# Performance work log

Measured on AMD Instinct MI355X. Metric: run time of the kernel, lower is better.

Reference implementation:

```python
import jax, jax.numpy as jnp
import numpy as np

N_NODES = 100000
N_EDGES = 1600000
N_GRAPHS = 128
IN_FEATS = 128
H2 = 128
N_CLASSES = 64


def setup_inputs() -> dict:
    key = jax.random.key(0)
    ks = jax.random.split(key, 12)
    return {
        "feat1": jax.random.normal(ks[0], (N_NODES, IN_FEATS), jnp.float32),
        "feat2": jax.random.normal(ks[1], (N_NODES, IN_FEATS), jnp.float32),
        "src1": jax.random.randint(ks[2], (N_EDGES,), 0, N_NODES),
        "dst1": jax.random.randint(ks[3], (N_EDGES,), 0, N_NODES),
        "gid1": jnp.sort(jax.random.randint(ks[4], (N_NODES,), 0, N_GRAPHS)),
        "src2": jax.random.randint(ks[5], (N_EDGES,), 0, N_NODES),
        "dst2": jax.random.randint(ks[6], (N_EDGES,), 0, N_NODES),
        "gid2": jnp.sort(jax.random.randint(ks[7], (N_NODES,), 0, N_GRAPHS)),
        "W": jax.random.normal(ks[8], (IN_FEATS, H2), jnp.float32) * 0.05,
        "b": jax.random.normal(ks[9], (H2,), jnp.float32) * 0.05,
        "Wc": jax.random.normal(ks[10], (H2, N_CLASSES), jnp.float32) * 0.05,
        "bc": jax.random.normal(ks[11], (N_CLASSES,), jnp.float32) * 0.05,
    }


def _gcn_branch(feat, src, dst, gid, W, b, Wc, bc):
    n = feat.shape[0]
    ones = jnp.ones(src.shape[0], feat.dtype)
    # DGL GraphConv norm='both': D_out^{-1/2} on src side, D_in^{-1/2} on dst side
    deg_out = jnp.clip(jax.ops.segment_sum(ones, src, num_segments=n), 1.0)
    deg_in = jnp.clip(jax.ops.segment_sum(ones, dst, num_segments=n), 1.0)
    h = feat * (deg_out ** -0.5)[:, None]
    h = h @ W  # project before aggregation (same linear math, fewer edge FLOPs)
    agg = jax.ops.segment_sum(h[src], dst, num_segments=n)  # [N, H2]
    h = agg * (deg_in ** -0.5)[:, None] + b
    # F.normalize (L2, dim=1, eps=1e-12) -> sigmoid -> relu (identity after sigmoid)
    h = h / jnp.clip(jnp.linalg.norm(h, axis=1, keepdims=True), 1e-12)
    h = jax.nn.relu(jax.nn.sigmoid(h))
    # dropout(0.3) omitted for deterministic reference (identity)
    # mean_nodes per graph
    hg = jax.ops.segment_sum(h, gid, num_segments=N_GRAPHS)
    cnt = jnp.clip(jax.ops.segment_sum(jnp.ones(n, h.dtype), gid, num_segments=N_GRAPHS), 1.0)
    hg = hg / cnt[:, None]
    return hg @ Wc + bc  # [G, C]


def reference(feat1, feat2, src1, dst1, gid1, src2, dst2, gid2, W, b, Wc, bc):
    h1 = _gcn_branch(feat1, src1, dst1, gid1, W, b, Wc, bc)
    h2 = _gcn_branch(feat2, src2, dst2, gid2, W, b, Wc, bc)
    # torch F.pairwise_distance: ||x1 - x2 + eps||_2 with eps=1e-6
    return jnp.linalg.norm(h1 - h2 + 1e-6, axis=1)
```

## Files before the change

### kernel.cpp

```cpp
#include <hip/hip_runtime.h>
#include <hip/hip_fp16.h>
#include <math.h>

#define F 128
#define C 64
#define G 128
#define KMAX 512
#define P1CH 2048
#define CAPB 4608

typedef _Float16 f16x8 __attribute__((ext_vector_type(8)));
typedef float f32x4 __attribute__((ext_vector_type(4)));

__device__ __forceinline__ void atomicAddF(float* p, float v) {
  __hip_atomic_fetch_add(p, v, __ATOMIC_RELAXED, __HIP_MEMORY_SCOPE_AGENT);
}

__global__ __launch_bounds__(256) void fscale_kernel(
    const float* __restrict__ feat1, const float* __restrict__ feat2,
    const float* __restrict__ dno1, const float* __restrict__ dno2,
    unsigned char* __restrict__ fs1, unsigned char* __restrict__ fs2, int N) {
  const float* feat = blockIdx.y ? feat2 : feat1;
  const float* dno = blockIdx.y ? dno2 : dno1;
  unsigned char* fs = blockIdx.y ? fs2 : fs1;
  int i = blockIdx.x * blockDim.x + threadIdx.x;
  if (i >= N * (F / 8)) return;
  int node = i >> 4;
  float dn = dno[node];
  float4 v0 = ((const float4*)feat)[i * 2];
  float4 v1 = ((const float4*)feat)[i * 2 + 1];
  int w0 = __builtin_amdgcn_cvt_pk_fp8_f32(v0.x * dn, v0.y * dn, 0, false);
  w0 = __builtin_amdgcn_cvt_pk_fp8_f32(v0.z * dn, v0.w * dn, w0, true);
  int w1 = __builtin_amdgcn_cvt_pk_fp8_f32(v1.x * dn, v1.y * dn, 0, false);
  w1 = __builtin_amdgcn_cvt_pk_fp8_f32(v1.z * dn, v1.w * dn, w1, true);
  uint2 pk;
  pk.x = (unsigned)w0;
  pk.y = (unsigned)w1;
  ((uint2*)fs)[i] = pk;
}

__global__ __launch_bounds__(256) void wconv_kernel(const float* __restrict__ Wg,
                                                    _Float16* __restrict__ Wt) {
  int tid = threadIdx.x;
#pragma unroll
  for (int i = 0; i < 8; ++i) {
    int f = tid + i * 256;
    int lane = f & 63;
    int ks = (f >> 6) & 3;
    int t = f >> 8;
    int n = t * 16 + (lane & 15);
    int k0 = ks * 32 + ((lane >> 4) << 3);
    f16x8 v;
#pragma unroll
    for (int j = 0; j < 8; ++j) v[j] = (_Float16)Wg[(k0 + j) * F + n];
    ((f16x8*)Wt)[f] = v;
  }
}

__global__ __launch_bounds__(128) void cnt_kernel(const int* __restrict__ gid1,
                                                  const int* __restrict__ gid2,
                                                  int* __restrict__ cnt1,
                                                  int* __restrict__ cnt2, int N) {
  const int* gid = blockIdx.x ? gid2 : gid1;
  int* cnt = blockIdx.x ? cnt2 : cnt1;
  int g = threadIdx.x;
  int lo = 0, hi = N;
  while (lo < hi) { int m = (lo + hi) >> 1; if (gid[m] < g) lo = m + 1; else hi = m; }
  int lo2 = lo, hi2 = N;
  while (lo2 < hi2) { int m = (lo2 + hi2) >> 1; if (gid[m] <= g) lo2 = m + 1; else hi2 = m; }
  cnt[g] = lo2 - lo;
}

__global__ __launch_bounds__(256) void pass1_kernel(
    const int* __restrict__ src1, const int* __restrict__ dst1,
    const int* __restrict__ src2, const int* __restrict__ dst2,
    int* __restrict__ bcntD1, int* __restrict__ bcntD2,
    int* __restrict__ bcntS1, int* __restrict__ bcntS2,
    unsigned* __restrict__ epkD1, unsigned* __restrict__ epkD2,
    unsigned char* __restrict__ epkS81, unsigned char* __restrict__ epkS82,
    int E, int K) {
  const int* src = blockIdx.y ? src2 : src1;
  const int* dst = blockIdx.y ? dst2 : dst1;
  int* bcntD = blockIdx.y ? bcntD2 : bcntD1;
  int* bcntS = blockIdx.y ? bcntS2 : bcntS1;
  unsigned* epkD = blockIdx.y ? epkD2 : epkD1;
  unsigned char* epkS8 = blockIdx.y ? epkS82 : epkS81;

  __shared__ int cntD[KMAX], resD[KMAX], baseD[KMAX];
  __shared__ int cntS[KMAX], resS[KMAX], baseS[KMAX];
  __shared__ unsigned stageD[P1CH];
  __shared__ unsigned char stageS[P1CH];
  __shared__ unsigned short bkD[P1CH];
  __shared__ unsigned short bkS[P1CH];

  int t = threadIdx.x;
  int lane = t & 63;
  int wv = t >> 6;

  for (int k = t; k < K; k += 256) { cntD[k] = 0; cntS[k] = 0; }
  __syncthreads();

  int e0 = blockIdx.x * P1CH;
  int e1 = e0 + P1CH; if (e1 > E) e1 = E;
  int M = e1 - e0;
  for (int i = e0 + t; i < e1; i += 256) {
    atomicAdd(&cntD[dst[i] >> 8], 1);
    atomicAdd(&cntS[src[i] >> 8], 1);
  }
  __syncthreads();

  if (wv == 0) {
    int carry = 0;
    for (int b0 = 0; b0 < K; b0 += 64) {
      int k = b0 + lane;
      int v = (k < K) ? cntD[k] : 0;
      int x = v;
#pragma unroll
      for (int off = 1; off < 64; off <<= 1) {
        int y = __shfl_up(x, off);
        if (lane >= off) x += y;
      }
      if (k < K) baseD[k] = carry + x - v;
      carry += __shfl(x, 63);
    }
  } else if (wv == 1) {
    int carry = 0;
    for (int b0 = 0; b0 < K; b0 += 64) {
      int k = b0 + lane;
      int v = (k < K) ? cntS[k] : 0;
      int x = v;
#pragma unroll
      for (int off = 1; off < 64; off <<= 1) {
        int y = __shfl_up(x, off);
        if (lane >= off) x += y;
      }
      if (k < K) baseS[k] = carry + x - v;
      carry += __shfl(x, 63);
    }
  }
  __syncthreads();

  for (int k = t; k < K; k += 256) {
    int c = cntD[k];
    resD[k] = c ? atomicAdd(&bcntD[k], c) : 0;
    int c2 = cntS[k];
    resS[k] = c2 ? atomicAdd(&bcntS[k], c2) : 0;
  }
  __syncthreads();

  for (int i = e0 + t; i < e1; i += 256) {
    int d = dst[i];
    int s = src[i];
    int kd = d >> 8;
    int p = atomicAdd(&baseD[kd], 1);
    stageD[p] = ((unsigned)(d & 255) << 24) | (unsigned)s;
    bkD[p] = (unsigned short)kd;
    int ks = s >> 8;
    int q = atomicAdd(&baseS[ks], 1);
    stageS[q] = (unsigned char)(s & 255);
    bkS[q] = (unsigned short)ks;
  }
  __syncthreads();

  for (int i = t; i < M; i += 256) {
    int bk = bkD[i];
    unsigned pos = (unsigned)(resD[bk] + (i - (baseD[bk] - cntD[bk])));
    if (pos < CAPB) epkD[(size_t)bk * CAPB + pos] = stageD[i];
  }
  for (int i = t; i < M; i += 256) {
    int bk = bkS[i];
    unsigned pos = (unsigned)(resS[bk] + (i - (baseS[bk] - cntS[bk])));
    if (pos < CAPB) epkS8[(size_t)bk * CAPB + pos] = stageS[i];
  }
}

__global__ __launch_bounds__(256) void pass2c_kernel(
    const int* __restrict__ bcntS1, const int* __restrict__ bcntS2,
    const unsigned char* __restrict__ epk1, const unsigned char* __restrict__ epk2,
    float* __restrict__ dno1, float* __restrict__ dno2, int N) {
  const int* bcntS = blockIdx.y ? bcntS2 : bcntS1;
  const unsigned char* epk = blockIdx.y ? epk2 : epk1;
  float* dno = blockIdx.y ? dno2 : dno1;

  __shared__ int lcnt[256];
  int b = blockIdx.x;
  int t = threadIdx.x;
  int s0 = b * CAPB;
  int M = bcntS[b]; if (M > CAPB) M = CAPB;
  lcnt[t] = 0;
  __syncthreads();
  for (int e = t; e < M; e += 256)
    atomicAdd(&lcnt[epk[s0 + e]], 1);
  __syncthreads();
  int node = (b << 8) + t;
  if (node < N) {
    int a = lcnt[t]; if (a < 1) a = 1;
    dno[node] = 1.0f / sqrtf((float)a);
  }
}

#define ACCP(rv)                                                        \
  do {                                                                  \
    auto f0 = __builtin_amdgcn_cvt_pk_f32_fp8((int)(rv).x, false);      \
    auto f1 = __builtin_amdgcn_cvt_pk_f32_fp8((int)(rv).x, true);       \
    auto f2 = __builtin_amdgcn_cvt_pk_f32_fp8((int)(rv).y, false);      \
    auto f3 = __builtin_amdgcn_cvt_pk_f32_fp8((int)(rv).y, true);       \
    a0.x += f0[0]; a0.y += f0[1]; a1.x += f1[0]; a1.y += f1[1];         \
    a2.x += f2[0]; a2.y += f2[1]; a3.x += f3[0]; a3.y += f3[1];         \
  } while (0)

__global__ __launch_bounds__(256) void p2g_kernel(
    const int* __restrict__ bcntD1, const int* __restrict__ bcntD2,
    const unsigned* __restrict__ epk1, const unsigned* __restrict__ epk2,
    int* __restrict__ degi1, int* __restrict__ degi2,
    const unsigned char* __restrict__ fs1, const unsigned char* __restrict__ fs2,
    __half* __restrict__ aggh1, __half* __restrict__ aggh2, int N) {
  const int* bcntD = blockIdx.y ? bcntD2 : bcntD1;
  const unsigned* epk = blockIdx.y ? epk2 : epk1;
  int* degi = blockIdx.y ? degi2 : degi1;
  const unsigned char* featsc = blockIdx.y ? fs2 : fs1;
  __half* aggh = blockIdx.y ? aggh2 : aggh1;

  __shared__ unsigned pk[CAPB];
  __shared__ unsigned srt[CAPB];
  __shared__ int lcnt[256];
  __shared__ int lcur[256];
  __shared__ int scur[256];

  int b = blockIdx.x;
  int t = threadIdx.x;
  size_t s0 = (size_t)b * CAPB;
  int M = bcntD[b]; if (M > CAPB) M = CAPB;

  lcnt[t] = 0;
  for (int e = t; e < M; e += 256) pk[e] = epk[s0 + e];
  __syncthreads();
  for (int e = t; e < M; e += 256) atomicAdd(&lcnt[pk[e] >> 24], 1);
  __syncthreads();

  int v = lcnt[t];
  lcur[t] = v;
  __syncthreads();
  for (int off = 1; off < 256; off <<= 1) {
    int x = (t >= off) ? lcur[t - off] : 0;
    __syncthreads();
    lcur[t] += x;
    __syncthreads();
  }
  int node = (b << 8) + t;
  if (node < N) degi[node] = v;
  scur[t] = lcur[t] - v;
  __syncthreads();

  for (int e = t; e < M; e += 256) {
    unsigned p = pk[e];
    int dl = p >> 24;
    int pos = atomicAdd(&scur[dl], 1);
    srt[pos] = p & 0xFFFFFFu;
  }
  __syncthreads();

  int g = t >> 4;
  int l = t & 15;
  const unsigned char* fl = featsc + l * 8;

  for (int nn = 0; nn < 16; ++nn) {
    int n = (g << 4) + nn;
    int node2 = (b << 8) + n;
    if (node2 >= N) break;
    int cnt = lcnt[n];
    int start = lcur[n] - cnt;

    float2 a0 = {0.f, 0.f}, a1 = {0.f, 0.f}, a2 = {0.f, 0.f}, a3 = {0.f, 0.f};

    for (int j0 = 0; j0 < cnt; j0 += 16) {
      int nb = cnt - j0; if (nb > 16) nb = 16;
      int myi = (l < nb) ? (int)srt[start + j0 + l] : 0;
      int k = 0;
      for (; k + 8 <= nb; k += 8) {
        int s0_ = __shfl(myi, k, 16);
        int s1_ = __shfl(myi, k + 1, 16);
        int s2_ = __shfl(myi, k + 2, 16);
        int s3_ = __shfl(myi, k + 3, 16);
        int s4_ = __shfl(myi, k + 4, 16);
        int s5_ = __shfl(myi, k + 5, 16);
        int s6_ = __shfl(myi, k + 6, 16);
        int s7_ = __shfl(myi, k + 7, 16);
        uint2 v0 = *(const uint2*)(fl + (size_t)s0_ * F);
        uint2 v1 = *(const uint2*)(fl + (size_t)s1_ * F);
        uint2 v2 = *(const uint2*)(fl + (size_t)s2_ * F);
        uint2 v3 = *(const uint2*)(fl + (size_t)s3_ * F);
        uint2 v4 = *(const uint2*)(fl + (size_t)s4_ * F);
        uint2 v5 = *(const uint2*)(fl + (size_t)s5_ * F);
        uint2 v6 = *(const uint2*)(fl + (size_t)s6_ * F);
        uint2 v7 = *(const uint2*)(fl + (size_t)s7_ * F);
        ACCP(v0);
        ACCP(v1);
        ACCP(v2);
        ACCP(v3);
        ACCP(v4);
        ACCP(v5);
        ACCP(v6);
        ACCP(v7);
      }
      for (; k + 4 <= nb; k += 4) {
        int s0_ = __shfl(myi, k, 16);
        int s1_ = __shfl(myi, k + 1, 16);
        int s2_ = __shfl(myi, k + 2, 16);
        int s3_ = __shfl(myi, k + 3, 16);
        uint2 v0 = *(const uint2*)(fl + (size_t)s0_ * F);
        uint2 v1 = *(const uint2*)(fl + (size_t)s1_ * F);
        uint2 v2 = *(const uint2*)(fl + (size_t)s2_ * F);
        uint2 v3 = *(const uint2*)(fl + (size_t)s3_ * F);
        ACCP(v0);
        ACCP(v1);
        ACCP(v2);
        ACCP(v3);
      }
      for (; k < nb; ++k) {
        int s_ = __shfl(myi, k, 16);
        uint2 vv = *(const uint2*)(fl + (size_t)s_ * F);
        ACCP(vv);
      }
    }

    f16x8 hv;
    hv[0] = (_Float16)a0.x; hv[1] = (_Float16)a0.y;
    hv[2] = (_Float16)a1.x; hv[3] = (_Float16)a1.y;
    hv[4] = (_Float16)a2.x; hv[5] = (_Float16)a2.y;
    hv[6] = (_Float16)a3.x; hv[7] = (_Float16)a3.y;
    __builtin_nontemporal_store(hv, (f16x8*)(aggh + (size_t)node2 * F) + l);
  }
}

__global__ __launch_bounds__(256) void gemm_epi_kernel(
    const __half* __restrict__ agg1, const int* __restrict__ degi1,
    const int* __restrict__ gid1, float* __restrict__ hg1,
    const __half* __restrict__ agg2, const int* __restrict__ degi2,
    const int* __restrict__ gid2, float* __restrict__ hg2,
    const _Float16* __restrict__ Wt, const float* __restrict__ bg, int N) {
  const __half* agg = blockIdx.y ? agg2 : agg1;
  const int* degi = blockIdx.y ? degi2 : degi1;
  const int* gid = blockIdx.y ? gid2 : gid1;
  float* hg = blockIdx.y ? hg2 : hg1;

  __shared__ __align__(16) _Float16 Wl[16384];
  __shared__ float hred[4][F];
  __shared__ int sgid[4];

  int tid = threadIdx.x;
  int wv = tid >> 6;
  int lane = tid & 63;
  int ln = lane & 15;
  int quad = lane >> 4;

  {
    const f16x8* src = (const f16x8*)Wt;
    f16x8* dst = (f16x8*)Wl;
#pragma unroll
    for (int i = 0; i < 8; ++i) dst[tid + i * 256] = src[tid + i * 256];
  }
  __syncthreads();

  int rbase = (blockIdx.x * 4 + wv) * 16;
  bool wave_active = rbase < N;

  int arow = rbase + ln; if (arow >= N) arow = N - 1;
  const _Float16* arow_p = (const _Float16*)(agg + (size_t)arow * F);
  f16x8 a[4];
#pragma unroll
  for (int ks = 0; ks < 4; ++ks)
    a[ks] = *(const f16x8*)(arow_p + ks * 32 + quad * 8);

  f32x4 acc[8];
#pragma unroll
  for (int t = 0; t < 8; ++t) acc[t] = (f32x4){0.f, 0.f, 0.f, 0.f};

#pragma unroll
  for (int t = 0; t < 8; ++t) {
#pragma unroll
    for (int ks = 0; ks < 4; ++ks) {
      f16x8 b = *(const f16x8*)&Wl[(((t << 2) + ks) * 64 + lane) * 8];
      acc[t] = __builtin_amdgcn_mfma_f32_16x16x32_f16(a[ks], b, acc[t], 0, 0, 0);
    }
  }

  float dnr[4]; int gg[4]; bool valid[4];
#pragma unroll
  for (int r = 0; r < 4; ++r) {
    int row = rbase + quad * 4 + r;
    valid[r] = row < N;
    int rc = valid[r] ? row : (N - 1);
    int dv = degi[rc]; if (dv < 1) dv = 1;
    dnr[r] = 1.0f / sqrtf((float)dv);
    gg[r] = gid[rc];
  }
  float bb[8];
#pragma unroll
  for (int t = 0; t < 8; ++t) bb[t] = bg[t * 16 + ln];

  float y[8][4], ssq[4];
#pragma unroll
  for (int r = 0; r < 4; ++r) ssq[r] = 0.f;
#pragma unroll
  for (int t = 0; t < 8; ++t) {
#pragma unroll
    for (int r = 0; r < 4; ++r) {
      float v = acc[t][r] * dnr[r] + bb[t];
      y[t][r] = v;
      ssq[r] += v * v;
    }
  }
#pragma unroll
  for (int m = 1; m < 16; m <<= 1) {
#pragma unroll
    for (int r = 0; r < 4; ++r) ssq[r] += __shfl_xor(ssq[r], m);
  }
  float u[8][4];
#pragma unroll
  for (int r = 0; r < 4; ++r) {
    float inv = 1.0f / fmaxf(sqrtf(ssq[r]), 1e-12f);
#pragma unroll
    for (int t = 0; t < 8; ++t) {
      float s = 1.0f / (1.0f + expf(-y[t][r] * inv));
      u[t][r] = valid[r] ? s : 0.0f;
    }
  }

  int rlast = rbase + 15; if (rlast >= N) rlast = N - 1;
  bool uniform = wave_active && (rbase + 15 < N) && (gid[rbase] == gid[rlast]);
  if (uniform) {
    float cs[8];
#pragma unroll
    for (int t = 0; t < 8; ++t) {
      cs[t] = u[t][0] + u[t][1] + u[t][2] + u[t][3];
      cs[t] += __shfl_xor(cs[t], 16);
      cs[t] += __shfl_xor(cs[t], 32);
    }
    if (lane == 0) sgid[wv] = gid[rbase];
    if (lane < 16) {
#pragma unroll
      for (int t = 0; t < 8; ++t) hred[wv][t * 16 + lane] = cs[t];
    }
  } else {
    if (lane == 0) sgid[wv] = -1;
    if (wave_active) {
#pragma unroll
      for (int r = 0; r < 4; ++r) {
        if (!valid[r]) continue;
#pragma unroll
        for (int t = 0; t < 8; ++t)
          atomicAddF(&hg[(size_t)gg[r] * F + t * 16 + ln], u[t][r]);
      }
    }
  }
  __syncthreads();
  if (tid < F) {
    int s0 = sgid[0], s1 = sgid[1], s2 = sgid[2], s3 = sgid[3];
    if (s0 >= 0 && s0 == s1 && s0 == s2 && s0 == s3) {
      atomicAddF(&hg[(size_t)s0 * F + tid],
                 hred[0][tid] + hred[1][tid] + hred[2][tid] + hred[3][tid]);
    } else {
      if (s0 >= 0) atomicAddF(&hg[(size_t)s0 * F + tid], hred[0][tid]);
      if (s1 >= 0) atomicAddF(&hg[(size_t)s1 * F + tid], hred[1][tid]);
      if (s2 >= 0) atomicAddF(&hg[(size_t)s2 * F + tid], hred[2][tid]);
      if (s3 >= 0) atomicAddF(&hg[(size_t)s3 * F + tid], hred[3][tid]);
    }
  }
}

__global__ __launch_bounds__(64) void final_kernel(
    const float* __restrict__ hg1, const int* __restrict__ cnt1,
    const float* __restrict__ hg2, const int* __restrict__ cnt2,
    const float* __restrict__ Wc, const float* __restrict__ bc,
    float* __restrict__ out) {
  __shared__ float v1[F], v2[F];
  int g = blockIdx.x, c = threadIdx.x;
  float ic1 = 1.0f / fmaxf((float)cnt1[g], 1.0f);
  float ic2 = 1.0f / fmaxf((float)cnt2[g], 1.0f);
  for (int i = c; i < F; i += 64) {
    v1[i] = hg1[(size_t)g * F + i] * ic1;
    v2[i] = hg2[(size_t)g * F + i] * ic2;
  }
  __syncthreads();
  float z1 = bc[c], z2 = bc[c];
  for (int k = 0; k < F; ++k) {
    float w = Wc[k * C + c];
    z1 += v1[k] * w;
    z2 += v2[k] * w;
  }
  float d = z1 - z2 + 1e-6f;
  d *= d;
#pragma unroll
  for (int m = 1; m < 64; m <<= 1) d += __shfl_xor(d, m);
  if (c == 0) out[g] = sqrtf(d);
}

extern "C" void kernel_launch(void* const* d_in, const int* in_sizes, int n_in,
                              void* d_out, int out_size, void* d_ws, size_t ws_size,
                              hipStream_t stream) {
  const float* feat1 = (const float*)d_in[0];
  const float* feat2 = (const float*)d_in[1];
  const int* src1 = (const int*)d_in[2];
  const int* dst1 = (const int*)d_in[3];
  const int* gid1 = (const int*)d_in[4];
  const int* src2 = (const int*)d_in[5];
  const int* dst2 = (const int*)d_in[6];
  const int* gid2 = (const int*)d_in[7];
  const float* Wg = (const float*)d_in[8];
  const float* bg = (const float*)d_in[9];
  const float* Wc = (const float*)d_in[10];
  const float* bc = (const float*)d_in[11];
  float* out = (float*)d_out;

  int N = in_sizes[0] / F;
  int E = in_sizes[2];
  int K = (N + 255) >> 8;
  if (K > KMAX) return;

  char* w = (char*)d_ws;
  float* hg1 = (float*)w; w += (size_t)G * F * 4;
  float* hg2 = (float*)w; w += (size_t)G * F * 4;
  int* bcntD1 = (int*)w; w += KMAX * 4;
  int* bcntD2 = (int*)w; w += KMAX * 4;
  int* bcntS1 = (int*)w; w += KMAX * 4;
  int* bcntS2 = (int*)w; w += KMAX * 4;
  size_t zbytes = (size_t)(w - (char*)d_ws);
  __half* aggh1 = (__half*)w; w += (size_t)N * F * 2;
  __half* aggh2 = (__half*)w; w += (size_t)N * F * 2;
  unsigned char* fs1 = (unsigned char*)w; w += (size_t)N * F;
  unsigned char* fs2 = (unsigned char*)w; w += (size_t)N * F;
  unsigned* epkD1 = (unsigned*)w; w += (size_t)K * CAPB * 4;
  unsigned* epkD2 = (unsigned*)w; w += (size_t)K * CAPB * 4;
  int* degi1 = (int*)w; w += (size_t)N * 4;
  int* degi2 = (int*)w; w += (size_t)N * 4;
  float* dno1 = (float*)w; w += (size_t)N * 4;
  float* dno2 = (float*)w; w += (size_t)N * 4;
  int* cnt1 = (int*)w; w += 128 * 4;
  int* cnt2 = (int*)w; w += 128 * 4;
  _Float16* Wt = (_Float16*)w; w += (size_t)F * F * 2;
  if ((size_t)(w - (char*)d_ws) > ws_size) return;

  unsigned char* epkS81 = (unsigned char*)aggh1;
  unsigned char* epkS82 = epkS81 + (size_t)K * CAPB;

  (void)hipMemsetAsync(d_ws, 0, zbytes, stream);

  wconv_kernel<<<1, 256, 0, stream>>>(Wg, Wt);
  cnt_kernel<<<2, 128, 0, stream>>>(gid1, gid2, cnt1, cnt2, N);

  int p1b = (E + P1CH - 1) / P1CH;
  pass1_kernel<<<dim3(p1b, 2), 256, 0, stream>>>(
      src1, dst1, src2, dst2, bcntD1, bcntD2, bcntS1, bcntS2,
      epkD1, epkD2, epkS81, epkS82, E, K);
  pass2c_kernel<<<dim3(K, 2), 256, 0, stream>>>(bcntS1, bcntS2, epkS81, epkS82,
                                                dno1, dno2, N);

  int fsb = (N * (F / 8) + 255) / 256;
  fscale_kernel<<<dim3(fsb, 2), 256, 0, stream>>>(feat1, feat2, dno1, dno2, fs1, fs2, N);

  p2g_kernel<<<dim3(K, 2), 256, 0, stream>>>(
      bcntD1, bcntD2, epkD1, epkD2, degi1, degi2, fs1, fs2, aggh1, aggh2, N);

  int gb = (N + 63) / 64;
  gemm_epi_kernel<<<dim3(gb, 2), 256, 0, stream>>>(
      aggh1, degi1, gid1, hg1, aggh2, degi2, gid2, hg2, Wt, bg, N);

  final_kernel<<<G, 64, 0, stream>>>(hg1, cnt1, hg2, cnt2, Wc, bc, out);
}
```

Before: 379.1 us.

## Pack bucket counters into padded 64-bit atomics and widen gather blocks to 512 threads

Combines the per-bucket dst and src counters into one 64-bit word, updated with a single atomic, and pads each to its own 64-byte slot to avoid false sharing between buckets. The gather kernel now runs 512 threads per bucket, so each 16-lane group handles 8 destination nodes instead of 16. That halves the serial node loop per group and adds more waves per block. The costs are extra idle threads in the 256-wide scan phases and possibly lower occupancy from the larger block.

```diff
diff --git a/kernel.cpp b/kernel.cpp
--- a/kernel.cpp
+++ b/kernel.cpp
@@ -74,15 +74,13 @@
 __global__ __launch_bounds__(256) void pass1_kernel(
     const int* __restrict__ src1, const int* __restrict__ dst1,
     const int* __restrict__ src2, const int* __restrict__ dst2,
-    int* __restrict__ bcntD1, int* __restrict__ bcntD2,
-    int* __restrict__ bcntS1, int* __restrict__ bcntS2,
+    unsigned long long* __restrict__ bcntDS1, unsigned long long* __restrict__ bcntDS2,
     unsigned* __restrict__ epkD1, unsigned* __restrict__ epkD2,
     unsigned char* __restrict__ epkS81, unsigned char* __restrict__ epkS82,
     int E, int K) {
   const int* src = blockIdx.y ? src2 : src1;
   const int* dst = blockIdx.y ? dst2 : dst1;
-  int* bcntD = blockIdx.y ? bcntD2 : bcntD1;
-  int* bcntS = blockIdx.y ? bcntS2 : bcntS1;
+  unsigned long long* bcntDS = blockIdx.y ? bcntDS2 : bcntDS1;
   unsigned* epkD = blockIdx.y ? epkD2 : epkD1;
   unsigned char* epkS8 = blockIdx.y ? epkS82 : epkS81;
 
@@ -142,9 +140,14 @@
 
   for (int k = t; k < K; k += 256) {
     int c = cntD[k];
-    resD[k] = c ? atomicAdd(&bcntD[k], c) : 0;
     int c2 = cntS[k];
-    resS[k] = c2 ? atomicAdd(&bcntS[k], c2) : 0;
+    if (c | c2) {
+      unsigned long long add =
+          (unsigned long long)(unsigned)c | ((unsigned long long)(unsigned)c2 << 32);
+      unsigned long long old = atomicAdd(&bcntDS[(size_t)k * 8], add);
+      resD[k] = (int)(old & 0xFFFFFFFFull);
+      resS[k] = (int)(old >> 32);
+    }
   }
   __syncthreads();
 
@@ -175,10 +178,11 @@
 }
 
 __global__ __launch_bounds__(256) void pass2c_kernel(
-    const int* __restrict__ bcntS1, const int* __restrict__ bcntS2,
+    const unsigned long long* __restrict__ bcntDS1,
+    const unsigned long long* __restrict__ bcntDS2,
     const unsigned char* __restrict__ epk1, const unsigned char* __restrict__ epk2,
     float* __restrict__ dno1, float* __restrict__ dno2, int N) {
-  const int* bcntS = blockIdx.y ? bcntS2 : bcntS1;
+  const unsigned long long* bcntDS = blockIdx.y ? bcntDS2 : bcntDS1;
   const unsigned char* epk = blockIdx.y ? epk2 : epk1;
   float* dno = blockIdx.y ? dno2 : dno1;
 
@@ -186,7 +190,7 @@
   int b = blockIdx.x;
   int t = threadIdx.x;
   int s0 = b * CAPB;
-  int M = bcntS[b]; if (M > CAPB) M = CAPB;
+  int M = (int)(bcntDS[(size_t)b * 8] >> 32); if (M > CAPB) M = CAPB;
   lcnt[t] = 0;
   __syncthreads();
   for (int e = t; e < M; e += 256)
@@ -209,13 +213,14 @@
     a2.x += f2[0]; a2.y += f2[1]; a3.x += f3[0]; a3.y += f3[1];         \
   } while (0)
 
-__global__ __launch_bounds__(256) void p2g_kernel(
-    const int* __restrict__ bcntD1, const int* __restrict__ bcntD2,
+__global__ __launch_bounds__(512) void p2g_kernel(
+    const unsigned long long* __restrict__ bcntDS1,
+    const unsigned long long* __restrict__ bcntDS2,
     const unsigned* __restrict__ epk1, const unsigned* __restrict__ epk2,
     int* __restrict__ degi1, int* __restrict__ degi2,
     const unsigned char* __restrict__ fs1, const unsigned char* __restrict__ fs2,
     __half* __restrict__ aggh1, __half* __restrict__ aggh2, int N) {
-  const int* bcntD = blockIdx.y ? bcntD2 : bcntD1;
+  const unsigned long long* bcntDS = blockIdx.y ? bcntDS2 : bcntDS1;
   const unsigned* epk = blockIdx.y ? epk2 : epk1;
   int* degi = blockIdx.y ? degi2 : degi1;
   const unsigned char* featsc = blockIdx.y ? fs2 : fs1;
@@ -230,29 +235,31 @@
   int b = blockIdx.x;
   int t = threadIdx.x;
   size_t s0 = (size_t)b * CAPB;
-  int M = bcntD[b]; if (M > CAPB) M = CAPB;
-
-  lcnt[t] = 0;
-  for (int e = t; e < M; e += 256) pk[e] = epk[s0 + e];
-  __syncthreads();
-  for (int e = t; e < M; e += 256) atomicAdd(&lcnt[pk[e] >> 24], 1);
-  __syncthreads();
-
-  int v = lcnt[t];
-  lcur[t] = v;
+  int M = (int)(bcntDS[(size_t)b * 8] & 0xFFFFFFFFull); if (M > CAPB) M = CAPB;
+
+  if (t < 256) lcnt[t] = 0;
+  for (int e = t; e < M; e += 512) pk[e] = epk[s0 + e];
+  __syncthreads();
+  for (int e = t; e < M; e += 512) atomicAdd(&lcnt[pk[e] >> 24], 1);
+  __syncthreads();
+
+  int v = (t < 256) ? lcnt[t] : 0;
+  if (t < 256) lcur[t] = v;
   __syncthreads();
   for (int off = 1; off < 256; off <<= 1) {
-    int x = (t >= off) ? lcur[t - off] : 0;
+    int x = (t < 256 && t >= off) ? lcur[t - off] : 0;
     __syncthreads();
-    lcur[t] += x;
+    if (t < 256) lcur[t] += x;
     __syncthreads();
   }
   int node = (b << 8) + t;
-  if (node < N) degi[node] = v;
-  scur[t] = lcur[t] - v;
-  __syncthreads();
-
-  for (int e = t; e < M; e += 256) {
+  if (t < 256) {
+    if (node < N) degi[node] = v;
+    scur[t] = lcur[t] - v;
+  }
+  __syncthreads();
+
+  for (int e = t; e < M; e += 512) {
     unsigned p = pk[e];
     int dl = p >> 24;
     int pos = atomicAdd(&scur[dl], 1);
@@ -264,8 +271,8 @@
   int l = t & 15;
   const unsigned char* fl = featsc + l * 8;
 
-  for (int nn = 0; nn < 16; ++nn) {
-    int n = (g << 4) + nn;
+  for (int nn = 0; nn < 8; ++nn) {
+    int n = (g << 3) + nn;
     int node2 = (b << 8) + n;
     if (node2 >= N) break;
     int cnt = lcnt[n];
@@ -521,10 +528,8 @@
   char* w = (char*)d_ws;
   float* hg1 = (float*)w; w += (size_t)G * F * 4;
   float* hg2 = (float*)w; w += (size_t)G * F * 4;
-  int* bcntD1 = (int*)w; w += KMAX * 4;
-  int* bcntD2 = (int*)w; w += KMAX * 4;
-  int* bcntS1 = (int*)w; w += KMAX * 4;
-  int* bcntS2 = (int*)w; w += KMAX * 4;
+  unsigned long long* bcntDS1 = (unsigned long long*)w; w += (size_t)KMAX * 64;
+  unsigned long long* bcntDS2 = (unsigned long long*)w; w += (size_t)KMAX * 64;
   size_t zbytes = (size_t)(w - (char*)d_ws);
   __half* aggh1 = (__half*)w; w += (size_t)N * F * 2;
   __half* aggh2 = (__half*)w; w += (size_t)N * F * 2;
@@ -551,16 +556,16 @@
 
   int p1b = (E + P1CH - 1) / P1CH;
   pass1_kernel<<<dim3(p1b, 2), 256, 0, stream>>>(
-      src1, dst1, src2, dst2, bcntD1, bcntD2, bcntS1, bcntS2,
+      src1, dst1, src2, dst2, bcntDS1, bcntDS2,
       epkD1, epkD2, epkS81, epkS82, E, K);
-  pass2c_kernel<<<dim3(K, 2), 256, 0, stream>>>(bcntS1, bcntS2, epkS81, epkS82,
+  pass2c_kernel<<<dim3(K, 2), 256, 0, stream>>>(bcntDS1, bcntDS2, epkS81, epkS82,
                                                 dno1, dno2, N);
 
   int fsb = (N * (F / 8) + 255) / 256;
   fscale_kernel<<<dim3(fsb, 2), 256, 0, stream>>>(feat1, feat2, dno1, dno2, fs1, fs2, N);
 
-  p2g_kernel<<<dim3(K, 2), 256, 0, stream>>>(
-      bcntD1, bcntD2, epkD1, epkD2, degi1, degi2, fs1, fs2, aggh1, aggh2, N);
+  p2g_kernel<<<dim3(K, 2), 512, 0, stream>>>(
+      bcntDS1, bcntDS2, epkD1, epkD2, degi1, degi2, fs1, fs2, aggh1, aggh2, N);
 
   int gb = (N + 63) / 64;
   gemm_epi_kernel<<<dim3(gb, 2), 256, 0, stream>>>(
```

Measured after the change: 409.3 us. 8.0% more time.
